# Kernel tuning notes

Hardware: AMD Instinct MI355X
Metric: run time of the kernel (lower is better)

## Reference

```python
import jax, jax.numpy as jnp
import numpy as np

N, E, T, B = 20000, 320000, 16, 32
IN, HID, LAT = 256, 512, 128

def _gelu(x):
    return jax.nn.gelu(x, approximate=False)  # torch F.gelu default = exact erf

def setup_inputs():
    key = jax.random.key(0)
    ks = jax.random.split(key, 20)
    s = 0.02
    f32 = jnp.float32
    return {
        "x_seq": jax.random.normal(ks[0], (T, N, IN), f32),
        "W1": jax.random.normal(ks[1], (IN, HID), f32) * s,
        "b1": jnp.zeros((HID,), f32),
        "W2": jax.random.normal(ks[2], (HID, HID), f32) * s,
        "b2": jnp.zeros((HID,), f32),
        "Wih0": jax.random.normal(ks[3], (4 * HID, HID), f32) * s,
        "Whh0": jax.random.normal(ks[4], (4 * HID, HID), f32) * s,
        "bih0": jnp.zeros((4 * HID,), f32),
        "bhh0": jnp.zeros((4 * HID,), f32),
        "Wih1": jax.random.normal(ks[5], (4 * HID, HID), f32) * s,
        "Whh1": jax.random.normal(ks[6], (4 * HID, HID), f32) * s,
        "bih1": jnp.zeros((4 * HID,), f32),
        "bhh1": jnp.zeros((4 * HID,), f32),
        "muW1": jax.random.normal(ks[7], (HID, HID), f32) * s,
        "mub1": jnp.zeros((HID,), f32),
        "muW2": jax.random.normal(ks[8], (HID, HID), f32) * s,
        "mub2": jnp.zeros((HID,), f32),
        "muW3": jax.random.normal(ks[9], (HID, LAT), f32) * s,
        "mub3": jnp.zeros((LAT,), f32),
        "lvW1": jax.random.normal(ks[10], (HID, HID), f32) * s,
        "lvb1": jnp.zeros((HID,), f32),
        "lvW2": jax.random.normal(ks[11], (HID, HID), f32) * s,
        "lvb2": jnp.zeros((HID,), f32),
        "lvW3": jax.random.normal(ks[12], (HID, LAT), f32) * s,
        "lvb3": jnp.zeros((LAT,), f32),
        "edge_index": jax.random.randint(ks[13], (2, E), 0, N),
        "batch": jnp.sort(jax.random.randint(ks[14], (N,), 0, B)),
    }

def _forward(x_seq, W1, b1, W2, b2, Wih0, Whh0, bih0, bhh0, Wih1, Whh1, bih1, bhh1,
             muW1, mub1, muW2, mub2, muW3, mub3, lvW1, lvb1, lvW2, lvb2, lvW3, lvb3,
             edge_index, batch):
    src, dst = edge_index[0], edge_index[1]
    loops = jnp.arange(N)
    src2 = jnp.concatenate([src, loops])  # PyG GCNConv adds self-loops by default
    dst2 = jnp.concatenate([dst, loops])
    deg = jax.ops.segment_sum(jnp.ones(E + N, x_seq.dtype), dst2, num_segments=N)
    dinv = jax.lax.rsqrt(deg)  # deg >= 1 due to self-loops
    norm = dinv[src2] * dinv[dst2]  # [E+N] symmetric normalization

    def conv(x, W, b):
        xw = x @ W  # dense transform first (GCNConv order)
        return jax.ops.segment_sum(norm[:, None] * xw[src2], dst2, num_segments=N) + b

    def gcn_step(carry, x_t):
        h = _gelu(conv(x_t, W1, b1))  # layer 0 + act (dropout p=0, eval)
        h = conv(h, W2, b2)           # final layer: no act
        return carry, jax.ops.segment_sum(h, batch, num_segments=B)  # global_add_pool

    _, pooled = jax.lax.scan(gcn_step, None, x_seq)  # [T, B, HID]
    seq = pooled.transpose(1, 0, 2)  # [B, T, HID] batch_first

    def lstm_layer(x, Wih, Whh, bih, bhh):
        H = Whh.shape[1]
        def step(carry, xt):
            h, c = carry
            g = xt @ Wih.T + h @ Whh.T + (bih + bhh)
            i, f, gg, o = jnp.split(g, 4, axis=-1)  # torch gate order i,f,g,o
            c2 = jax.nn.sigmoid(f) * c + jax.nn.sigmoid(i) * jnp.tanh(gg)
            h2 = jax.nn.sigmoid(o) * jnp.tanh(c2)
            return (h2, c2), h2
        z0 = jnp.zeros((x.shape[0], H), x.dtype)
        _, ys = jax.lax.scan(step, (z0, z0), x.transpose(1, 0, 2))
        return ys.transpose(1, 0, 2)

    out = lstm_layer(seq, Wih0, Whh0, bih0, bhh0)
    out = lstm_layer(out, Wih1, Whh1, bih1, bhh1)
    final = out[:, -1, :]  # [B, HID] last timestep hidden

    def mlp(h, Wa, ba, Wb, bb, Wc, bc):
        h = _gelu(h @ Wa + ba)
        h = _gelu(h @ Wb + bb)
        return h @ Wc + bc

    mu = mlp(final, muW1, mub1, muW2, mub2, muW3, mub3)
    logvar = jnp.minimum(mlp(final, lvW1, lvb1, lvW2, lvb2, lvW3, lvb3), 10.0)
    z = mu  # eval mode: z = mu (no reparameterization noise)
    return mu, logvar, z

def reference(x_seq, W1, b1, W2, b2, Wih0, Whh0, bih0, bhh0, Wih1, Whh1, bih1, bhh1,
              muW1, mub1, muW2, mub2, muW3, mub3, lvW1, lvb1, lvW2, lvb2, lvW3, lvb3,
              edge_index, batch):
    return _forward(x_seq, W1, b1, W2, b2, Wih0, Whh0, bih0, bhh0, Wih1, Whh1, bih1, bhh1,
                    muW1, mub1, muW2, mub2, muW3, mub3, lvW1, lvb1, lvW2, lvb2, lvW3, lvb3,
                    edge_index, batch)
```

## Files before the change

### kernel.cpp

```cpp
#include <hip/hip_runtime.h>
#include <math.h>

#define T_STEPS 16
#define NB 32
#define D_IN 256
#define D_HID 512
#define D_LAT 128

static __device__ __forceinline__ float gelu_f(float x){
  return 0.5f * x * (1.0f + erff(x * 0.70710678118654752440f));
}
static __device__ __forceinline__ float sigm_f(float x){
  return 1.0f / (1.0f + expf(-x));
}

__global__ void k_count(const int* __restrict__ dst, int E, int* __restrict__ counts){
  int e = blockIdx.x*256 + threadIdx.x;
  if (e < E) atomicAdd(&counts[dst[e]], 1);
}

__global__ void k_dinv(const int* __restrict__ counts, float* __restrict__ dinv, int n){
  int i = blockIdx.x*256 + threadIdx.x;
  if (i < n) dinv[i] = 1.0f / sqrtf((float)(counts[i] + 1));
}

__global__ void k_scan(const int* __restrict__ counts, int* __restrict__ row_ptr, int n){
  __shared__ int sm[1024];
  __shared__ int carry;
  if (threadIdx.x == 0) carry = 0;
  __syncthreads();
  for (int base = 0; base < n; base += 1024){
    int i = base + threadIdx.x;
    int v = (i < n) ? counts[i] : 0;
    sm[threadIdx.x] = v;
    __syncthreads();
    for (int off = 1; off < 1024; off <<= 1){
      int t = (threadIdx.x >= off) ? sm[threadIdx.x - off] : 0;
      __syncthreads();
      sm[threadIdx.x] += t;
      __syncthreads();
    }
    if (i < n) row_ptr[i] = carry + sm[threadIdx.x] - v;
    int total = sm[1023];
    __syncthreads();
    if (threadIdx.x == 0) carry += total;
    __syncthreads();
  }
  if (threadIdx.x == 0) row_ptr[n] = carry;
}

__global__ void k_place(const int* __restrict__ src, const int* __restrict__ dst,
                        const int* __restrict__ row_ptr, int* __restrict__ fill,
                        int* __restrict__ csr_col, int E){
  int e = blockIdx.x*256 + threadIdx.x;
  if (e < E){
    int d = dst[e];
    int p = row_ptr[d] + atomicAdd(&fill[d], 1);
    csr_col[p] = src[e];
  }
}

__global__ void k_ps_edges(const int* __restrict__ src, const int* __restrict__ dst,
                           const int* __restrict__ batch, const float* __restrict__ dinv,
                           float* __restrict__ ps, int E, int n){
  int e = blockIdx.x*256 + threadIdx.x;
  if (e < E){
    int s = src[e], d = dst[e];
    atomicAdd(&ps[(size_t)batch[d]*n + s], dinv[s]*dinv[d]);
  }
}

__global__ void k_ps_self(const int* __restrict__ batch, const float* __restrict__ dinv,
                          float* __restrict__ ps, float* __restrict__ cntb, int n){
  int i = blockIdx.x*256 + threadIdx.x;
  if (i < n){
    ps[(size_t)batch[i]*n + i] += dinv[i]*dinv[i];
    atomicAdd(&cntb[batch[i]], 1.0f);
  }
}

__global__ __launch_bounds__(256) void k_spmm(const float* __restrict__ x, const float* __restrict__ dinv,
                       const int* __restrict__ row_ptr, const int* __restrict__ csr_col,
                       float* __restrict__ sx, int n){
  int i = blockIdx.x*4 + (threadIdx.x >> 6);
  int lane = threadIdx.x & 63;
  if (i >= n) return;
  const float4* x4 = (const float4*)x;
  float di = dinv[i];
  float4 a = x4[(size_t)i*64 + lane];
  float4 acc = make_float4(di*a.x, di*a.y, di*a.z, di*a.w);
  int e0 = row_ptr[i], e1 = row_ptr[i+1];
  for (int e = e0; e < e1; ++e){
    int c = csr_col[e];
    float w = dinv[c];
    float4 v = x4[(size_t)c*64 + lane];
    acc.x += w*v.x; acc.y += w*v.y; acc.z += w*v.z; acc.w += w*v.w;
  }
  acc.x *= di; acc.y *= di; acc.z *= di; acc.w *= di;
  ((float4*)sx)[(size_t)i*64 + lane] = acc;
}

__global__ __launch_bounds__(256) void k_gemm_gelu(const float* __restrict__ A, const float* __restrict__ B,
                            const float* __restrict__ bias, float* __restrict__ C, int M){
  __shared__ float As[32][68];
  __shared__ float Bs[32][64];
  int bm = blockIdx.x * 64;
  int bn = blockIdx.y * 64;
  int tid = threadIdx.x;
  int tx = tid & 15, ty = tid >> 4;
  float acc[4][4] = {{0.f}};
  for (int k0 = 0; k0 < 256; k0 += 32){
    for (int s = tid; s < 512; s += 256){
      int row = s >> 3, c4 = s & 7;
      int gr = bm + row;
      float4 v = make_float4(0.f,0.f,0.f,0.f);
      if (gr < M) v = *(const float4*)(A + (size_t)gr*256 + k0 + c4*4);
      As[c4*4+0][row] = v.x; As[c4*4+1][row] = v.y; As[c4*4+2][row] = v.z; As[c4*4+3][row] = v.w;
    }
    for (int s = tid; s < 512; s += 256){
      int row = s >> 4, c4 = s & 15;
      *(float4*)(&Bs[row][c4*4]) = *(const float4*)(B + (size_t)(k0+row)*512 + bn + c4*4);
    }
    __syncthreads();
    #pragma unroll
    for (int kk = 0; kk < 32; ++kk){
      float4 av = *(const float4*)(&As[kk][ty*4]);
      float4 bv = *(const float4*)(&Bs[kk][tx*4]);
      float a[4] = {av.x, av.y, av.z, av.w};
      float b[4] = {bv.x, bv.y, bv.z, bv.w};
      #pragma unroll
      for (int i=0;i<4;++i)
        #pragma unroll
        for (int j=0;j<4;++j) acc[i][j] += a[i]*b[j];
    }
    __syncthreads();
  }
  #pragma unroll
  for (int i=0;i<4;++i){
    int row = bm + ty*4 + i;
    if (row < M){
      #pragma unroll
      for (int j=0;j<4;++j){
        int col = bn + tx*4 + j;
        C[(size_t)row*512 + col] = gelu_f(acc[i][j] + bias[col]);
      }
    }
  }
}

__global__ __launch_bounds__(256) void k_pool(const float* __restrict__ ps, const float* __restrict__ h1,
                       float* __restrict__ pp, int n){
  __shared__ float pss[32][65];
  int tid = threadIdx.x;
  int tx = tid & 127, ty = tid >> 7;
  int k0 = blockIdx.x * 512;
  int n0 = blockIdx.y * 128;
  float acc[16];
  #pragma unroll
  for (int m=0;m<16;++m) acc[m] = 0.f;
  for (int kc=0; kc<512; kc+=64){
    int kb = k0 + kc;
    for (int s=tid; s<2048; s+=256){
      int m = s >> 6, kk = s & 63;
      int gk = kb + kk;
      pss[m][kk] = (gk < n) ? ps[(size_t)m*n + gk] : 0.f;
    }
    __syncthreads();
    int kmax = n - kb; if (kmax > 64) kmax = 64; if (kmax < 0) kmax = 0;
    for (int kk=0; kk<kmax; ++kk){
      float hv = h1[(size_t)(kb+kk)*512 + n0 + tx];
      #pragma unroll
      for (int m=0;m<16;++m) acc[m] += pss[ty*16+m][kk]*hv;
    }
    __syncthreads();
  }
  #pragma unroll
  for (int m=0;m<16;++m) atomicAdd(&pp[(size_t)(ty*16+m)*512 + n0 + tx], acc[m]);
}

__global__ void k_seq(const float* __restrict__ pp_all, const float* __restrict__ W2,
                      const float* __restrict__ b2, const float* __restrict__ cntb,
                      float* __restrict__ seq){
  int g = blockIdx.x*256 + threadIdx.x;
  int k = g & 511;
  int bt = g >> 9;
  int b = bt >> 4, t = bt & 15;
  const float* pr = pp_all + (size_t)(t*NB + b)*512;
  float acc = cntb[b]*b2[k];
  for (int j=0;j<512;++j) acc += pr[j]*W2[(size_t)j*512+k];
  seq[g] = acc;
}

__global__ void k_transpose(const float* __restrict__ in, float* __restrict__ out, int R, int C){
  __shared__ float tile[32][33];
  int c0 = blockIdx.x*32, r0 = blockIdx.y*32;
  int tx = threadIdx.x, ty = threadIdx.y;
  for (int j=0;j<32;j+=8){
    tile[ty+j][tx] = in[(size_t)(r0+ty+j)*C + c0 + tx];
  }
  __syncthreads();
  for (int j=0;j<32;j+=8){
    out[(size_t)(c0+ty+j)*R + r0 + tx] = tile[tx][ty+j];
  }
}

__global__ __launch_bounds__(256) void k_xg(const float* __restrict__ in, const float* __restrict__ WT,
                     const float* __restrict__ bih, const float* __restrict__ bhh,
                     float* __restrict__ xg){
  __shared__ float ins[8][512];
  int jg = blockIdx.x & 7, btg = blockIdx.x >> 3;
  int tid = threadIdx.x;
  int j = jg*256 + tid;
  const float4* in4 = (const float4*)(in + (size_t)btg*8*512);
  float4* ins4 = (float4*)ins;
  for (int s=tid; s<1024; s+=256) ins4[s] = in4[s];
  __syncthreads();
  float bb = bih[j] + bhh[j];
  float acc[8];
  #pragma unroll
  for (int r=0;r<8;++r) acc[r] = bb;
  for (int kk=0; kk<512; ++kk){
    float w = WT[(size_t)kk*2048 + j];
    #pragma unroll
    for (int r=0;r<8;++r) acc[r] += ins[r][kk]*w;
  }
  for (int r=0;r<8;++r) xg[(size_t)(btg*8+r)*2048 + j] = acc[r];
}

__global__ __launch_bounds__(256) void k_lstm_step(const float* __restrict__ xg, const float* __restrict__ WhhT,
                            const float* __restrict__ h_in, float* __restrict__ h_out,
                            float* __restrict__ c, float* __restrict__ ys, int t){
  __shared__ float hs[8][512];
  int kg = blockIdx.x & 15, bg = blockIdx.x >> 4;
  int tid = threadIdx.x;
  int tb = tid >> 5, tk = tid & 31;
  const float4* h4 = (const float4*)(h_in + (size_t)bg*8*512);
  float4* hs4 = (float4*)hs;
  for (int s=tid; s<1024; s+=256) hs4[s] = h4[s];
  __syncthreads();
  int b = bg*8 + tb;
  int k = kg*32 + tk;
  const float* xgr = xg + (size_t)(b*T_STEPS + t)*2048;
  float gi = xgr[k], gf = xgr[k+512], gg = xgr[k+1024], go = xgr[k+1536];
  for (int kk=0; kk<512; ++kk){
    float hv = hs[tb][kk];
    const float* wr = WhhT + (size_t)kk*2048;
    gi += hv*wr[k];
    gf += hv*wr[k+512];
    gg += hv*wr[k+1024];
    go += hv*wr[k+1536];
  }
  float cold = c[(size_t)b*512+k];
  float c2 = sigm_f(gf)*cold + sigm_f(gi)*tanhf(gg);
  float h2 = sigm_f(go)*tanhf(c2);
  c[(size_t)b*512+k] = c2;
  h_out[(size_t)b*512+k] = h2;
  if (ys) ys[(size_t)(b*T_STEPS + t)*512 + k] = h2;
}

__global__ void k_head(const float* __restrict__ A, const float* __restrict__ W,
                       const float* __restrict__ bias, float* __restrict__ out,
                       int K, int Nc, int mode, float* __restrict__ out2){
  int g = blockIdx.x*256 + threadIdx.x;
  if (g >= 32*Nc) return;
  int b = g / Nc, k = g % Nc;
  const float* ar = A + (size_t)b*K;
  float acc = bias[k];
  for (int j=0;j<K;++j) acc += ar[j]*W[(size_t)j*Nc+k];
  if (mode == 1) acc = gelu_f(acc);
  else if (mode == 2) acc = fminf(acc, 10.0f);
  out[g] = acc;
  if (out2) out2[g] = acc;
}

extern "C" void kernel_launch(void* const* d_in, const int* in_sizes, int n_in,
                              void* d_out, int out_size, void* d_ws, size_t ws_size,
                              hipStream_t stream){
  const float* x_seq = (const float*)d_in[0];
  const float* W1   = (const float*)d_in[1];
  const float* b1   = (const float*)d_in[2];
  const float* W2   = (const float*)d_in[3];
  const float* b2   = (const float*)d_in[4];
  const float* Wih0 = (const float*)d_in[5];
  const float* Whh0 = (const float*)d_in[6];
  const float* bih0 = (const float*)d_in[7];
  const float* bhh0 = (const float*)d_in[8];
  const float* Wih1 = (const float*)d_in[9];
  const float* Whh1 = (const float*)d_in[10];
  const float* bih1 = (const float*)d_in[11];
  const float* bhh1 = (const float*)d_in[12];
  const float* muW1 = (const float*)d_in[13];
  const float* mub1 = (const float*)d_in[14];
  const float* muW2 = (const float*)d_in[15];
  const float* mub2 = (const float*)d_in[16];
  const float* muW3 = (const float*)d_in[17];
  const float* mub3 = (const float*)d_in[18];
  const float* lvW1 = (const float*)d_in[19];
  const float* lvb1 = (const float*)d_in[20];
  const float* lvW2 = (const float*)d_in[21];
  const float* lvb2 = (const float*)d_in[22];
  const float* lvW3 = (const float*)d_in[23];
  const float* lvb3 = (const float*)d_in[24];
  const int* edge_index = (const int*)d_in[25];
  const int* batch      = (const int*)d_in[26];
  int E = in_sizes[25] / 2;
  int N = in_sizes[26];
  const int* src = edge_index;
  const int* dst = edge_index + E;
  (void)n_in; (void)out_size; (void)ws_size;

  char* w = (char*)d_ws;
  size_t off = 0;
  auto carve = [&](size_t bytes)->void*{
    void* p = w + off;
    off = (off + bytes + 255) & ~(size_t)255;
    return p;
  };

  float* dinv    = (float*)carve((size_t)N*4);
  int*   counts  = (int*)  carve((size_t)N*4);
  int*   row_ptr = (int*)  carve((size_t)(N+1)*4);
  int*   fillb   = (int*)  carve((size_t)N*4);
  int*   csr_col = (int*)  carve((size_t)E*4);
  float* ps      = (float*)carve((size_t)NB*N*4);
  float* cntb    = (float*)carve((size_t)NB*4);
  float* sx      = (float*)carve((size_t)N*256*4);
  float* h1buf   = (float*)carve((size_t)N*512*4);
  float* pp_all  = (float*)carve((size_t)T_STEPS*NB*512*4);
  float* seqb    = (float*)carve((size_t)NB*T_STEPS*512*4);
  float* WT_ih   = (float*)carve((size_t)512*2048*4);
  float* WT_hh   = (float*)carve((size_t)512*2048*4);
  float* xg      = (float*)carve((size_t)NB*T_STEPS*2048*4);
  float* ys0     = (float*)carve((size_t)NB*T_STEPS*512*4);
  float* h0b     = (float*)carve((size_t)NB*512*4);
  float* h1b     = (float*)carve((size_t)NB*512*4);
  float* cb      = (float*)carve((size_t)NB*512*4);
  float* t1      = (float*)carve((size_t)NB*512*4);
  float* t2      = (float*)carve((size_t)NB*512*4);

  hipMemsetAsync(counts, 0, (size_t)N*4, stream);
  hipMemsetAsync(fillb, 0, (size_t)N*4, stream);
  hipMemsetAsync(ps, 0, (size_t)NB*N*4, stream);
  hipMemsetAsync(cntb, 0, (size_t)NB*4, stream);
  hipMemsetAsync(pp_all, 0, (size_t)T_STEPS*NB*512*4, stream);

  int gE = (E + 255)/256, gN = (N + 255)/256;
  k_count<<<gE,256,0,stream>>>(dst, E, counts);
  k_dinv<<<gN,256,0,stream>>>(counts, dinv, N);
  k_scan<<<1,1024,0,stream>>>(counts, row_ptr, N);
  k_place<<<gE,256,0,stream>>>(src, dst, row_ptr, fillb, csr_col, E);
  k_ps_edges<<<gE,256,0,stream>>>(src, dst, batch, dinv, ps, E, N);
  k_ps_self<<<gN,256,0,stream>>>(batch, dinv, ps, cntb, N);

  dim3 gemm_grid((N+63)/64, 8);
  dim3 pool_grid((N+511)/512, 4);
  for (int t=0; t<T_STEPS; ++t){
    k_spmm<<<(N+3)/4,256,0,stream>>>(x_seq + (size_t)t*N*256, dinv, row_ptr, csr_col, sx, N);
    k_gemm_gelu<<<gemm_grid,256,0,stream>>>(sx, W1, b1, h1buf, N);
    k_pool<<<pool_grid,256,0,stream>>>(ps, h1buf, pp_all + (size_t)t*NB*512, N);
  }
  k_seq<<<(512*512)/256,256,0,stream>>>(pp_all, W2, b2, cntb, seqb);

  dim3 tr_grid(16, 64), tr_blk(32, 8);
  k_transpose<<<tr_grid,tr_blk,0,stream>>>(Wih0, WT_ih, 2048, 512);
  k_transpose<<<tr_grid,tr_blk,0,stream>>>(Whh0, WT_hh, 2048, 512);
  k_xg<<<512,256,0,stream>>>(seqb, WT_ih, bih0, bhh0, xg);
  hipMemsetAsync(h0b, 0, (size_t)NB*512*4, stream);
  hipMemsetAsync(cb, 0, (size_t)NB*512*4, stream);
  for (int t=0;t<T_STEPS;++t){
    float* hin  = (t & 1) ? h1b : h0b;
    float* hout = (t & 1) ? h0b : h1b;
    k_lstm_step<<<64,256,0,stream>>>(xg, WT_hh, hin, hout, cb, ys0, t);
  }
  k_transpose<<<tr_grid,tr_blk,0,stream>>>(Wih1, WT_ih, 2048, 512);
  k_transpose<<<tr_grid,tr_blk,0,stream>>>(Whh1, WT_hh, 2048, 512);
  k_xg<<<512,256,0,stream>>>(ys0, WT_ih, bih1, bhh1, xg);
  hipMemsetAsync(h0b, 0, (size_t)NB*512*4, stream);
  hipMemsetAsync(cb, 0, (size_t)NB*512*4, stream);
  for (int t=0;t<T_STEPS;++t){
    float* hin  = (t & 1) ? h1b : h0b;
    float* hout = (t & 1) ? h0b : h1b;
    k_lstm_step<<<64,256,0,stream>>>(xg, WT_hh, hin, hout, cb, (float*)nullptr, t);
  }
  float* fin = h0b;

  float* mu_out = (float*)d_out;
  float* lv_out = mu_out + 32*128;
  float* z_out  = mu_out + 2*32*128;
  k_head<<<64,256,0,stream>>>(fin, muW1, mub1, t1, 512, 512, 1, (float*)nullptr);
  k_head<<<64,256,0,stream>>>(t1, muW2, mub2, t2, 512, 512, 1, (float*)nullptr);
  k_head<<<16,256,0,stream>>>(t2, muW3, mub3, mu_out, 512, 128, 0, z_out);
  k_head<<<64,256,0,stream>>>(fin, lvW1, lvb1, t1, 512, 512, 1, (float*)nullptr);
  k_head<<<64,256,0,stream>>>(t1, lvW2, lvb2, t2, 512, 512, 1, (float*)nullptr);
  k_head<<<16,256,0,stream>>>(t2, lvW3, lvb3, lv_out, 512, 128, 2, (float*)nullptr);
}
```

Before: 6.342 ms.

## Replace fp32 SIMT GEMM with split-bf16 MFMA GEMM using direct LDS loads

```diff
diff --git a/kernel.cpp b/kernel.cpp
--- a/kernel.cpp
+++ b/kernel.cpp
@@ -7,11 +7,24 @@
 #define D_HID 512
 #define D_LAT 128
 
+typedef __attribute__((ext_vector_type(8))) short bf16x8_t;
+typedef __attribute__((ext_vector_type(4))) float f32x4_t;
+
 static __device__ __forceinline__ float gelu_f(float x){
   return 0.5f * x * (1.0f + erff(x * 0.70710678118654752440f));
 }
 static __device__ __forceinline__ float sigm_f(float x){
   return 1.0f / (1.0f + expf(-x));
+}
+static __device__ __forceinline__ unsigned short bf16_rn(float x){
+  unsigned int u = __float_as_uint(x);
+  unsigned int r = (u + 0x7FFFu + ((u >> 16) & 1u)) >> 16;
+  return (unsigned short)r;
+}
+static __device__ __forceinline__ void split2(float x, unsigned short& hi, unsigned short& lo){
+  hi = bf16_rn(x);
+  float hf = __uint_as_float(((unsigned int)hi) << 16);
+  lo = bf16_rn(x - hf);
 }
 
 __global__ void k_count(const int* __restrict__ dst, int E, int* __restrict__ counts){
@@ -79,9 +92,19 @@
   }
 }
 
+__global__ void k_prepB(const float* __restrict__ W1, unsigned short* __restrict__ B3T){
+  int g = blockIdx.x*256 + threadIdx.x;
+  if (g >= 256*512) return;
+  int kc = g >> 9, n = g & 511;
+  unsigned short hi, lo;
+  split2(W1[(size_t)kc*512 + n], hi, lo);
+  unsigned short* r = B3T + (size_t)n*768;
+  r[kc] = hi; r[256+kc] = lo; r[512+kc] = hi;
+}
+
 __global__ __launch_bounds__(256) void k_spmm(const float* __restrict__ x, const float* __restrict__ dinv,
                        const int* __restrict__ row_ptr, const int* __restrict__ csr_col,
-                       float* __restrict__ sx, int n){
+                       unsigned short* __restrict__ A2, int n){
   int i = blockIdx.x*4 + (threadIdx.x >> 6);
   int lane = threadIdx.x & 63;
   if (i >= n) return;
@@ -97,52 +120,76 @@
     acc.x += w*v.x; acc.y += w*v.y; acc.z += w*v.z; acc.w += w*v.w;
   }
   acc.x *= di; acc.y *= di; acc.z *= di; acc.w *= di;
-  ((float4*)sx)[(size_t)i*64 + lane] = acc;
-}
-
-__global__ __launch_bounds__(256) void k_gemm_gelu(const float* __restrict__ A, const float* __restrict__ B,
+  ushort4 h4, l4;
+  split2(acc.x, h4.x, l4.x); split2(acc.y, h4.y, l4.y);
+  split2(acc.z, h4.z, l4.z); split2(acc.w, h4.w, l4.w);
+  *(ushort4*)(A2 + (size_t)i*512 + lane*4)       = h4;
+  *(ushort4*)(A2 + (size_t)i*512 + 256 + lane*4) = l4;
+}
+
+__global__ __launch_bounds__(256) void k_gemm_mfma(const unsigned short* __restrict__ A2,
+                            const unsigned short* __restrict__ B3T,
                             const float* __restrict__ bias, float* __restrict__ C, int M){
-  __shared__ float As[32][68];
-  __shared__ float Bs[32][64];
-  int bm = blockIdx.x * 64;
-  int bn = blockIdx.y * 64;
+  __shared__ __align__(16) unsigned short As[128*32];
+  __shared__ __align__(16) unsigned short Bs[128*32];
+  int bm = blockIdx.x * 128;
+  int bn = blockIdx.y * 128;
   int tid = threadIdx.x;
-  int tx = tid & 15, ty = tid >> 4;
-  float acc[4][4] = {{0.f}};
-  for (int k0 = 0; k0 < 256; k0 += 32){
-    for (int s = tid; s < 512; s += 256){
-      int row = s >> 3, c4 = s & 7;
-      int gr = bm + row;
-      float4 v = make_float4(0.f,0.f,0.f,0.f);
-      if (gr < M) v = *(const float4*)(A + (size_t)gr*256 + k0 + c4*4);
-      As[c4*4+0][row] = v.x; As[c4*4+1][row] = v.y; As[c4*4+2][row] = v.z; As[c4*4+3][row] = v.w;
-    }
-    for (int s = tid; s < 512; s += 256){
-      int row = s >> 4, c4 = s & 15;
-      *(float4*)(&Bs[row][c4*4]) = *(const float4*)(B + (size_t)(k0+row)*512 + bn + c4*4);
-    }
-    __syncthreads();
-    #pragma unroll
-    for (int kk = 0; kk < 32; ++kk){
-      float4 av = *(const float4*)(&As[kk][ty*4]);
-      float4 bv = *(const float4*)(&Bs[kk][tx*4]);
-      float a[4] = {av.x, av.y, av.z, av.w};
-      float b[4] = {bv.x, bv.y, bv.z, bv.w};
+  int wave = tid >> 6, lane = tid & 63;
+  int wr = (wave >> 1) * 64, wc = (wave & 1) * 64;
+  int m16 = lane & 15, g = lane >> 4;
+
+  f32x4_t acc[4][4];
+  #pragma unroll
+  for (int i=0;i<4;++i)
+    #pragma unroll
+    for (int j=0;j<4;++j) acc[i][j] = (f32x4_t){0.f,0.f,0.f,0.f};
+
+  for (int s = 0; s < 24; ++s){
+    int seg = s >> 3, kc = (s & 7) * 32;
+    int acol = (seg == 2) ? (256 + kc) : kc;
+    int bcol = s * 32;
+    #pragma unroll
+    for (int i = 0; i < 2; ++i){
+      int c = i*256 + tid;
+      int row = c >> 2, cb = (c & 3) * 8;
+      const unsigned short* aSrc = A2 + (size_t)(bm + row)*512 + acol + cb;
+      const unsigned short* bSrc = B3T + (size_t)(bn + row)*768 + bcol + cb;
+      unsigned short* aDst = (unsigned short*)As + (size_t)(i*256 + wave*64)*8;
+      unsigned short* bDst = (unsigned short*)Bs + (size_t)(i*256 + wave*64)*8;
+      __builtin_amdgcn_global_load_lds((const __attribute__((address_space(1))) void*)aSrc,
+                                       (__attribute__((address_space(3))) void*)aDst, 16, 0, 0);
+      __builtin_amdgcn_global_load_lds((const __attribute__((address_space(1))) void*)bSrc,
+                                       (__attribute__((address_space(3))) void*)bDst, 16, 0, 0);
+    }
+    __syncthreads();
+    bf16x8_t af[4], bf[4];
+    #pragma unroll
+    for (int f=0; f<4; ++f){
+      af[f] = *(const bf16x8_t*)(As + ((wr + f*16 + m16)*32 + g*8));
+      bf[f] = *(const bf16x8_t*)(Bs + ((wc + f*16 + m16)*32 + g*8));
+    }
+    #pragma unroll
+    for (int fi=0; fi<4; ++fi)
       #pragma unroll
-      for (int i=0;i<4;++i)
-        #pragma unroll
-        for (int j=0;j<4;++j) acc[i][j] += a[i]*b[j];
-    }
-    __syncthreads();
-  }
+      for (int fj=0; fj<4; ++fj)
+        acc[fi][fj] = __builtin_amdgcn_mfma_f32_16x16x32_bf16(af[fi], bf[fj], acc[fi][fj], 0, 0, 0);
+    __syncthreads();
+  }
+
   #pragma unroll
-  for (int i=0;i<4;++i){
-    int row = bm + ty*4 + i;
-    if (row < M){
+  for (int fi=0; fi<4; ++fi){
+    #pragma unroll
+    for (int fj=0; fj<4; ++fj){
+      int col = bn + wc + fj*16 + m16;
+      float bv = bias[col];
       #pragma unroll
-      for (int j=0;j<4;++j){
-        int col = bn + tx*4 + j;
-        C[(size_t)row*512 + col] = gelu_f(acc[i][j] + bias[col]);
+      for (int r=0; r<4; ++r){
+        int row = bm + wr + fi*16 + g*4 + r;
+        if (row < M){
+          float v = acc[fi][fj][r] + bv;
+          C[(size_t)row*512 + col] = gelu_f(v);
+        }
       }
     }
   }
@@ -309,6 +356,8 @@
   const int* dst = edge_index + E;
   (void)n_in; (void)out_size; (void)ws_size;
 
+  int Mp = ((N + 127) & ~127);
+
   char* w = (char*)d_ws;
   size_t off = 0;
   auto carve = [&](size_t bytes)->void*{
@@ -324,7 +373,8 @@
   int*   csr_col = (int*)  carve((size_t)E*4);
   float* ps      = (float*)carve((size_t)NB*N*4);
   float* cntb    = (float*)carve((size_t)NB*4);
-  float* sx      = (float*)carve((size_t)N*256*4);
+  unsigned short* A2  = (unsigned short*)carve((size_t)Mp*512*2);
+  unsigned short* B3T = (unsigned short*)carve((size_t)512*768*2);
   float* h1buf   = (float*)carve((size_t)N*512*4);
   float* pp_all  = (float*)carve((size_t)T_STEPS*NB*512*4);
   float* seqb    = (float*)carve((size_t)NB*T_STEPS*512*4);
@@ -343,6 +393,7 @@
   hipMemsetAsync(ps, 0, (size_t)NB*N*4, stream);
   hipMemsetAsync(cntb, 0, (size_t)NB*4, stream);
   hipMemsetAsync(pp_all, 0, (size_t)T_STEPS*NB*512*4, stream);
+  hipMemsetAsync(A2 + (size_t)N*512, 0, (size_t)(Mp - N)*512*2, stream);
 
   int gE = (E + 255)/256, gN = (N + 255)/256;
   k_count<<<gE,256,0,stream>>>(dst, E, counts);
@@ -351,12 +402,13 @@
   k_place<<<gE,256,0,stream>>>(src, dst, row_ptr, fillb, csr_col, E);
   k_ps_edges<<<gE,256,0,stream>>>(src, dst, batch, dinv, ps, E, N);
   k_ps_self<<<gN,256,0,stream>>>(batch, dinv, ps, cntb, N);
-
-  dim3 gemm_grid((N+63)/64, 8);
+  k_prepB<<<512,256,0,stream>>>(W1, B3T);
+
+  dim3 gemm_grid(Mp/128, 4);
   dim3 pool_grid((N+511)/512, 4);
   for (int t=0; t<T_STEPS; ++t){
-    k_spmm<<<(N+3)/4,256,0,stream>>>(x_seq + (size_t)t*N*256, dinv, row_ptr, csr_col, sx, N);
-    k_gemm_gelu<<<gemm_grid,256,0,stream>>>(sx, W1, b1, h1buf, N);
+    k_spmm<<<(N+3)/4,256,0,stream>>>(x_seq + (size_t)t*N*256, dinv, row_ptr, csr_col, A2, N);
+    k_gemm_mfma<<<gemm_grid,256,0,stream>>>(A2, B3T, b1, h1buf, N);
     k_pool<<<pool_grid,256,0,stream>>>(ps, h1buf, pp_all + (size_t)t*NB*512, N);
   }
   k_seq<<<(512*512)/256,256,0,stream>>>(pp_all, W2, b2, cntb, seqb);
```

After: 5.677 ms. 1.12x faster.
